# Optimization experiments

Measured on AMD Instinct MI355X. Metric: run time of the kernel, lower is better.

The kernel has to match this reference:

```python
import jax, jax.numpy as jnp
import numpy as np

N_NODES = 100000


def gcn_conv(x, edge_index, W, b):
    # PyG GCNConv: add self-loops, symmetric norm, then scatter-aggregate.
    n = x.shape[0]
    x = x @ W  # [N, out]
    src = jnp.concatenate([edge_index[0], jnp.arange(n)])  # self-loops
    dst = jnp.concatenate([edge_index[1], jnp.arange(n)])
    ones = jnp.ones(src.shape[0], dtype=x.dtype)
    deg = jax.ops.segment_sum(ones, dst, num_segments=n)  # in-degree incl. self-loops
    dis = jnp.where(deg > 0, jax.lax.rsqrt(deg), 0.0)
    norm = dis[src] * dis[dst]  # [E+N]
    msg = x[src] * norm[:, None]  # gather + scale
    out = jax.ops.segment_sum(msg, dst, num_segments=n)
    return out + b


def setup_inputs() -> dict:
    key = jax.random.key(0)
    ks = jax.random.split(key, 8)
    in_dim, h1, h2, out_dim, E = 128, 128, 64, 10, 1600000
    glorot = lambda k, fi, fo: jax.random.normal(k, (fi, fo), jnp.float32) * np.sqrt(2.0 / (fi + fo))
    return {
        "x": jax.random.normal(ks[0], (N_NODES, in_dim), jnp.float32),
        "edge_index": jax.random.randint(ks[1], (2, E), 0, N_NODES, jnp.int64),
        "W1": glorot(ks[2], in_dim, h1),
        "b1": jnp.zeros((h1,), jnp.float32),
        "W2": glorot(ks[3], h1, h2),
        "b2": jnp.zeros((h2,), jnp.float32),
        "Wf": glorot(ks[4], h2, out_dim),
        "bf": jnp.zeros((out_dim,), jnp.float32),
    }


def reference(x, edge_index, W1, b1, W2, b2, Wf, bf):
    h = jax.nn.relu(gcn_conv(x, edge_index, W1, b1))
    h = jax.nn.relu(gcn_conv(h, edge_index, W2, b2))
    logits = h @ Wf + bf
    return jax.nn.softmax(logits, axis=1)
```

## Files before the change

kernel.cpp:

```cpp
#include <hip/hip_runtime.h>
#include <math.h>

#define NN 100000
#define D_IN 128
#define D_H1 128
#define D_H2 64
#define D_O 10
#define NB 256
#define BDIV 391
#define ECH 4096
#define COLCAP 8192

static const size_t OFF_G1     = 0;
static const size_t OFF_G2     = 25600000;
static const size_t OFF_W1T    = 40000000;
static const size_t OFF_W2T    = 40100000;
static const size_t OFF_PART   = 76800000;
static const size_t OFF_COL    = 102400000;
static const size_t OFF_DIS    = 108800000;
static const size_t OFF_ROWPTR = 109300000;
static const size_t OFF_HIST   = 109800000;
static const size_t OFF_TOT    = 110700000;

typedef __attribute__((ext_vector_type(8))) short short8;
typedef __attribute__((ext_vector_type(4))) float floatx4;

__device__ inline unsigned int pack_bf2(float a, float b) {
  unsigned int ua = __float_as_uint(a);
  ua += 0x7fffu + ((ua >> 16) & 1u);
  unsigned int ub = __float_as_uint(b);
  ub += 0x7fffu + ((ub >> 16) & 1u);
  return (ua >> 16) | (ub & 0xffff0000u);
}
__device__ inline unsigned short bf16u(float a) {
  unsigned int ua = __float_as_uint(a);
  ua += 0x7fffu + ((ua >> 16) & 1u);
  return (unsigned short)(ua >> 16);
}
__device__ inline float bflo(unsigned int u) { return __uint_as_float(u << 16); }
__device__ inline float bfhi(unsigned int u) { return __uint_as_float(u & 0xffff0000u); }
__device__ inline short8 as_short8(uint4 u) {
  union { uint4 u4; short8 s8; } c; c.u4 = u; return c.s8;
}
__device__ inline void acc_u4(float* acc, uint4 u) {
  acc[0] += bflo(u.x); acc[1] += bfhi(u.x);
  acc[2] += bflo(u.y); acc[3] += bfhi(u.y);
  acc[4] += bflo(u.z); acc[5] += bfhi(u.z);
  acc[6] += bflo(u.w); acc[7] += bfhi(u.w);
}

__global__ __launch_bounds__(256) void histo_kernel(
    const int* __restrict__ dst, int* __restrict__ H, int E, int nchunk,
    const float* __restrict__ W1, const float* __restrict__ W2,
    unsigned short* __restrict__ w1t, unsigned short* __restrict__ w2t) {
  __shared__ int hist[NB];
  const int tid = threadIdx.x;
  hist[tid] = 0;
  __syncthreads();
  const int e0 = blockIdx.x * ECH;
#pragma unroll
  for (int i = 0; i < ECH / 256; ++i) {
    int e = e0 + i * 256 + tid;
    if (e < E) atomicAdd(&hist[dst[e] / BDIV], 1);
  }
  __syncthreads();
  H[tid * nchunk + blockIdx.x] = hist[tid];
  if (blockIdx.x < 64) {
    int o = blockIdx.x * 256 + tid;
    int nn = o >> 7, k = o & 127;
    w1t[o] = bf16u(W1[(size_t)k * D_H1 + nn]);
  } else if (blockIdx.x < 96) {
    int o = (blockIdx.x - 64) * 256 + tid;
    int nn = o >> 7, k = o & 127;
    w2t[o] = bf16u(W2[(size_t)k * D_H2 + nn]);
  }
}

__global__ __launch_bounds__(256) void bucket_scan_kernel(
    int* __restrict__ H, int* __restrict__ total, int nchunk) {
  __shared__ int sm[256];
  const int tid = threadIdx.x;
  int* row = H + (size_t)blockIdx.x * nchunk;
  int carry = 0;
  for (int t0 = 0; t0 < nchunk; t0 += 256) {
    int idx = t0 + tid;
    int v = (idx < nchunk) ? row[idx] : 0;
    sm[tid] = v;
    __syncthreads();
#pragma unroll
    for (int off = 1; off < 256; off <<= 1) {
      int t2 = (tid >= off) ? sm[tid - off] : 0;
      __syncthreads();
      sm[tid] += t2;
      __syncthreads();
    }
    int incl = sm[tid];
    int ttot = sm[255];
    __syncthreads();
    if (idx < nchunk) row[idx] = carry + incl - v;
    carry += ttot;
  }
  if (tid == 0) total[blockIdx.x] = carry;
}

__global__ __launch_bounds__(256) void scatter_kernel(
    const int* __restrict__ src, const int* __restrict__ dst,
    const int* __restrict__ H, const int* __restrict__ total,
    unsigned int* __restrict__ part, int E, int nchunk) {
  __shared__ int sm[NB];
  __shared__ int offs_s[NB];
  __shared__ int base_s[NB];
  __shared__ int cnt[NB];
  const int tid = threadIdx.x;
  {
    int v = total[tid];
    sm[tid] = v;
    __syncthreads();
#pragma unroll
    for (int off = 1; off < 256; off <<= 1) {
      int t2 = (tid >= off) ? sm[tid - off] : 0;
      __syncthreads();
      sm[tid] += t2;
      __syncthreads();
    }
    base_s[tid] = sm[tid] - v;
  }
  offs_s[tid] = H[tid * nchunk + blockIdx.x];
  cnt[tid] = 0;
  __syncthreads();
  const int e0 = blockIdx.x * ECH;
#pragma unroll
  for (int i = 0; i < ECH / 256; ++i) {
    int e = e0 + i * 256 + tid;
    if (e < E) {
      int d = dst[e];
      int s = src[e];
      int b = d / BDIV;
      int r = atomicAdd(&cnt[b], 1);
      unsigned int p = ((unsigned int)(d - b * BDIV) << 17) | (unsigned int)s;
      part[(size_t)base_s[b] + offs_s[b] + r] = p;
    }
  }
}

__global__ __launch_bounds__(256) void bucket_csr_kernel(
    const unsigned int* __restrict__ part, const int* __restrict__ total,
    int* __restrict__ row_ptr, float* __restrict__ dis,
    int* __restrict__ col, int n, int E) {
  __shared__ int sm[256];
  __shared__ int ldeg[BDIV + 1];
  __shared__ int lofs[BDIV + 1];
  __shared__ int col_s[COLCAP];
  __shared__ int ebase_s, ecnt_s;
  const int tid = threadIdx.x;
  const int b = blockIdx.x;
  const int lo = b * BDIV;
  const int nn = min(n - lo, BDIV);
  {
    int v = total[tid];
    sm[tid] = v;
    __syncthreads();
#pragma unroll
    for (int off = 1; off < 256; off <<= 1) {
      int t2 = (tid >= off) ? sm[tid - off] : 0;
      __syncthreads();
      sm[tid] += t2;
      __syncthreads();
    }
    if (tid == b) { ebase_s = sm[tid] - v; ecnt_s = v; }
  }
  for (int t = tid; t <= BDIV; t += 256) ldeg[t] = 0;
  __syncthreads();
  const int ebase = ebase_s;
  const int ecnt = ecnt_s;
  for (int i0 = 0; i0 < ecnt; i0 += 256) {
    int idx = i0 + tid;
    if (idx < ecnt) atomicAdd(&ldeg[part[ebase + idx] >> 17], 1);
  }
  __syncthreads();
  int carry = 0;
  for (int t0 = 0; t0 < BDIV + 1; t0 += 256) {
    int idx = t0 + tid;
    int v = (idx <= BDIV) ? ldeg[idx] : 0;
    sm[tid] = v;
    __syncthreads();
#pragma unroll
    for (int off = 1; off < 256; off <<= 1) {
      int t2 = (tid >= off) ? sm[tid - off] : 0;
      __syncthreads();
      sm[tid] += t2;
      __syncthreads();
    }
    int incl = sm[tid];
    int ttot = sm[255];
    __syncthreads();
    if (idx <= BDIV) lofs[idx] = carry + incl - v;
    carry += ttot;
  }
  __syncthreads();
  for (int t = tid; t < nn; t += 256) {
    row_ptr[lo + t] = ebase + lofs[t];
    dis[lo + t] = rsqrtf((float)ldeg[t] + 1.0f);
  }
  if (b == NB - 1 && tid == 0) row_ptr[n] = E;
  __syncthreads();
  for (int i0 = 0; i0 < ecnt; i0 += 256) {
    int idx = i0 + tid;
    if (idx < ecnt) {
      unsigned int p = part[ebase + idx];
      int r = atomicAdd(&lofs[p >> 17], 1);
      if (r < COLCAP) col_s[r] = (int)(p & 0x1FFFFu);
    }
  }
  __syncthreads();
  const int m = min(ecnt, COLCAP);
  for (int idx = tid; idx < m; idx += 256) col[ebase + idx] = col_s[idx];
}

template <int NOUT>
__global__ __launch_bounds__(256) void gemm_mfma_kernel(
    const float* __restrict__ A_, const unsigned short* __restrict__ wt,
    const float* __restrict__ dis, unsigned short* __restrict__ out, int nrows) {
  constexpr int K = 128;
  constexpr int NT = NOUT / 16;
  constexpr int LDW = K + 8;
  __shared__ unsigned short buf[4 * 16 * LDW];
  const int tid = threadIdx.x;

  const int wave = tid >> 6;
  const int lane = tid & 63;
  const int quad = lane >> 4;
  const int cg = lane & 15;
  const int row0w = blockIdx.x * 64 + wave * 16;

  short8 afr[4];
  {
    int row = row0w + cg;
    if (row > nrows - 1) row = nrows - 1;
#pragma unroll
    for (int kb = 0; kb < 4; ++kb) {
      const float* p = A_ + (size_t)row * K + kb * 32 + quad * 8;
      float4 v0 = *(const float4*)(p);
      float4 v1 = *(const float4*)(p + 4);
      uint4 u;
      u.x = pack_bf2(v0.x, v0.y); u.y = pack_bf2(v0.z, v0.w);
      u.z = pack_bf2(v1.x, v1.y); u.w = pack_bf2(v1.z, v1.w);
      afr[kb] = as_short8(u);
    }
  }

  floatx4 acc[NT];
#pragma unroll
  for (int t = 0; t < NT; ++t) acc[t] = (floatx4){0.f, 0.f, 0.f, 0.f};
#pragma unroll
  for (int t = 0; t < NT; ++t) {
    const unsigned short* wrow = wt + (size_t)(t * 16 + cg) * K;
#pragma unroll
    for (int kb = 0; kb < 4; ++kb) {
      short8 bfr = *(const short8*)(wrow + kb * 32 + quad * 8);
      acc[t] = __builtin_amdgcn_mfma_f32_16x16x32_bf16(afr[kb], bfr, acc[t], 0, 0, 0);
    }
  }

  float4 dv4 = *(const float4*)(dis + row0w + quad * 4);
  float dvs[4] = {dv4.x, dv4.y, dv4.z, dv4.w};
  unsigned short* mybuf = buf + wave * 16 * LDW;
#pragma unroll
  for (int t = 0; t < NT; ++t)
#pragma unroll
    for (int r = 0; r < 4; ++r)
      mybuf[(quad * 4 + r) * LDW + t * 16 + cg] = bf16u(acc[t][r] * dvs[r]);
  __syncthreads();

  constexpr int CHUNKS = NOUT / 8;
  constexpr int RPI = 64 / CHUNKS;
  int cid = lane % CHUNKS;
  int rs = lane / CHUNKS;
#pragma unroll
  for (int i = 0; i < 16 / RPI; ++i) {
    int r = rs + i * RPI;
    int grow = row0w + r;
    if (grow < nrows) {
      uint4 u = *(const uint4*)(mybuf + r * LDW + cid * 8);
      *(uint4*)(out + (size_t)grow * NOUT + cid * 8) = u;
    }
  }
}

__global__ __launch_bounds__(256, 8) void gather1_gemm2_kernel(
    const unsigned short* __restrict__ g, const int* __restrict__ col,
    const int* __restrict__ row_ptr, const float* __restrict__ dis,
    const float* __restrict__ b1, const unsigned short* __restrict__ w2t,
    unsigned short* __restrict__ g2, int n) {
  constexpr int K = D_H1;
  constexpr int LDW = K + 8;
  constexpr int LDO = 80;
  __shared__ unsigned short hl[16 * LDW];
  __shared__ unsigned short obuf[16 * LDO];
  const int tid = threadIdx.x;
  const int row0 = blockIdx.x * 16;

  {
    const int v = row0 + (tid >> 4);
    const int c = (tid & 15) * 8;
    const int start = row_ptr[v];
    const int end = row_ptr[v + 1];
    float acc[8];
#pragma unroll
    for (int q = 0; q < 8; ++q) acc[q] = 0.f;
    acc_u4(acc, *(const uint4*)(g + (size_t)v * K + c));
    int e = start;
    for (; e + 4 <= end; e += 4) {
      int s0 = col[e + 0], s1 = col[e + 1], s2 = col[e + 2], s3 = col[e + 3];
      uint4 u0 = *(const uint4*)(g + (size_t)s0 * K + c);
      uint4 u1 = *(const uint4*)(g + (size_t)s1 * K + c);
      uint4 u2 = *(const uint4*)(g + (size_t)s2 * K + c);
      uint4 u3 = *(const uint4*)(g + (size_t)s3 * K + c);
      acc_u4(acc, u0); acc_u4(acc, u1); acc_u4(acc, u2); acc_u4(acc, u3);
    }
    for (; e < end; ++e) {
      uint4 u = *(const uint4*)(g + (size_t)col[e] * K + c);
      acc_u4(acc, u);
    }
    float dv = dis[v];
    float4 bv0 = *(const float4*)(b1 + c);
    float4 bv1 = *(const float4*)(b1 + c + 4);
    float r0 = fmaxf(dv * acc[0] + bv0.x, 0.f);
    float r1 = fmaxf(dv * acc[1] + bv0.y, 0.f);
    float r2 = fmaxf(dv * acc[2] + bv0.z, 0.f);
    float r3 = fmaxf(dv * acc[3] + bv0.w, 0.f);
    float r4 = fmaxf(dv * acc[4] + bv1.x, 0.f);
    float r5 = fmaxf(dv * acc[5] + bv1.y, 0.f);
    float r6 = fmaxf(dv * acc[6] + bv1.z, 0.f);
    float r7 = fmaxf(dv * acc[7] + bv1.w, 0.f);
    uint4 o;
    o.x = pack_bf2(r0, r1);
    o.y = pack_bf2(r2, r3);
    o.z = pack_bf2(r4, r5);
    o.w = pack_bf2(r6, r7);
    *(uint4*)(hl + (tid >> 4) * LDW + c) = o;
  }
  __syncthreads();

  {
    const int wave = tid >> 6;
    const int lane = tid & 63;
    const int quad = lane >> 4;
    const int cg = lane & 15;
    floatx4 acc = (floatx4){0.f, 0.f, 0.f, 0.f};
    const unsigned short* wrow = w2t + (size_t)(wave * 16 + cg) * K;
    const unsigned short* arow = hl + cg * LDW;
#pragma unroll
    for (int kb = 0; kb < 4; ++kb) {
      short8 afr = *(const short8*)(arow + kb * 32 + quad * 8);
      short8 bfr = *(const short8*)(wrow + kb * 32 + quad * 8);
      acc = __builtin_amdgcn_mfma_f32_16x16x32_bf16(afr, bfr, acc, 0, 0, 0);
    }
    float4 dv4 = *(const float4*)(dis + row0 + quad * 4);
    float dvs[4] = {dv4.x, dv4.y, dv4.z, dv4.w};
#pragma unroll
    for (int r = 0; r < 4; ++r)
      obuf[(quad * 4 + r) * LDO + wave * 16 + cg] = bf16u(acc[r] * dvs[r]);
  }
  __syncthreads();

  if (tid < 128) {
    int r = tid >> 3;
    int cid = tid & 7;
    uint4 u = *(const uint4*)(obuf + r * LDO + cid * 8);
    *(uint4*)(g2 + (size_t)(row0 + r) * D_H2 + cid * 8) = u;
  }
}

__global__ __launch_bounds__(256) void gather2_final_kernel(
    const unsigned short* __restrict__ g, const int* __restrict__ col,
    const int* __restrict__ row_ptr, const float* __restrict__ dis,
    const float* __restrict__ b2, const float* __restrict__ Wf,
    const float* __restrict__ bf, float* __restrict__ out, int n) {
  constexpr int LDH = 72;
  __shared__ unsigned short ha[32 * LDH];
  __shared__ unsigned short wtf[16 * LDH];
  __shared__ float bfs[D_O];
  __shared__ float ls[32][12];
  const int tid = threadIdx.x;
  if (tid < 128) {
    int nn = tid >> 3;
    int k = (tid & 7) * 8;
    uint4 u;
    if (nn < D_O) {
      u.x = pack_bf2(Wf[(size_t)(k + 0) * D_O + nn], Wf[(size_t)(k + 1) * D_O + nn]);
      u.y = pack_bf2(Wf[(size_t)(k + 2) * D_O + nn], Wf[(size_t)(k + 3) * D_O + nn]);
      u.z = pack_bf2(Wf[(size_t)(k + 4) * D_O + nn], Wf[(size_t)(k + 5) * D_O + nn]);
      u.w = pack_bf2(Wf[(size_t)(k + 6) * D_O + nn], Wf[(size_t)(k + 7) * D_O + nn]);
    } else {
      u = make_uint4(0u, 0u, 0u, 0u);
    }
    *(uint4*)(wtf + nn * LDH + k) = u;
  }
  if (tid < D_O) bfs[tid] = bf[tid];

  const int gid = blockIdx.x * 256 + tid;
  const int v = gid >> 3;
  const int nl = tid >> 3;
  const int c = (tid & 7) * 8;
  if (v < n) {
    int start = row_ptr[v];
    int end = row_ptr[v + 1];
    float acc[8];
#pragma unroll
    for (int q = 0; q < 8; ++q) acc[q] = 0.f;
    acc_u4(acc, *(const uint4*)(g + (size_t)v * D_H2 + c));
    int e = start;
    for (; e + 4 <= end; e += 4) {
      int s0 = col[e + 0], s1 = col[e + 1], s2 = col[e + 2], s3 = col[e + 3];
      uint4 u0 = *(const uint4*)(g + (size_t)s0 * D_H2 + c);
      uint4 u1 = *(const uint4*)(g + (size_t)s1 * D_H2 + c);
      uint4 u2 = *(const uint4*)(g + (size_t)s2 * D_H2 + c);
      uint4 u3 = *(const uint4*)(g + (size_t)s3 * D_H2 + c);
      acc_u4(acc, u0); acc_u4(acc, u1); acc_u4(acc, u2); acc_u4(acc, u3);
    }
    for (; e < end; ++e) {
      uint4 u = *(const uint4*)(g + (size_t)col[e] * D_H2 + c);
      acc_u4(acc, u);
    }
    float dv = dis[v];
    float4 bv0 = *(const float4*)(b2 + c);
    float4 bv1 = *(const float4*)(b2 + c + 4);
    float r0 = fmaxf(dv * acc[0] + bv0.x, 0.f);
    float r1 = fmaxf(dv * acc[1] + bv0.y, 0.f);
    float r2 = fmaxf(dv * acc[2] + bv0.z, 0.f);
    float r3 = fmaxf(dv * acc[3] + bv0.w, 0.f);
    float r4 = fmaxf(dv * acc[4] + bv1.x, 0.f);
    float r5 = fmaxf(dv * acc[5] + bv1.y, 0.f);
    float r6 = fmaxf(dv * acc[6] + bv1.z, 0.f);
    float r7 = fmaxf(dv * acc[7] + bv1.w, 0.f);
    uint4 o;
    o.x = pack_bf2(r0, r1);
    o.y = pack_bf2(r2, r3);
    o.z = pack_bf2(r4, r5);
    o.w = pack_bf2(r6, r7);
    *(uint4*)(ha + nl * LDH + c) = o;
  }
  __syncthreads();
  {
    const int wave = tid >> 6;
    if (wave < 2) {
      const int lane = tid & 63;
      const int quad = lane >> 4;
      const int cg = lane & 15;
      floatx4 acc = (floatx4){0.f, 0.f, 0.f, 0.f};
      const unsigned short* arow = ha + (wave * 16 + cg) * LDH;
      const unsigned short* wrow = wtf + cg * LDH;
#pragma unroll
      for (int kb = 0; kb < 2; ++kb) {
        short8 afr = *(const short8*)(arow + kb * 32 + quad * 8);
        short8 bfr = *(const short8*)(wrow + kb * 32 + quad * 8);
        acc = __builtin_amdgcn_mfma_f32_16x16x32_bf16(afr, bfr, acc, 0, 0, 0);
      }
      if (cg < D_O) {
        float bb = bfs[cg];
#pragma unroll
        for (int r = 0; r < 4; ++r)
          ls[wave * 16 + quad * 4 + r][cg] = acc[r] + bb;
      }
    }
  }
  __syncthreads();
  if (tid < 32) {
    int v2 = blockIdx.x * 32 + tid;
    if (v2 < n) {
      float m = ls[tid][0];
#pragma unroll
      for (int j = 1; j < D_O; ++j) m = fmaxf(m, ls[tid][j]);
      float s = 0.f;
      float ex[D_O];
#pragma unroll
      for (int j = 0; j < D_O; ++j) { ex[j] = expf(ls[tid][j] - m); s += ex[j]; }
      float inv = 1.0f / s;
#pragma unroll
      for (int j = 0; j < D_O; ++j) ls[tid][j] = ex[j] * inv;
    }
  }
  __syncthreads();
  for (int idx = tid; idx < 32 * D_O; idx += 256) {
    int gidx = blockIdx.x * 32 * D_O + idx;
    if (gidx < n * D_O) out[gidx] = ls[idx / D_O][idx % D_O];
  }
}

extern "C" void kernel_launch(void* const* d_in, const int* in_sizes, int n_in,
                              void* d_out, int out_size, void* d_ws, size_t ws_size,
                              hipStream_t stream) {
  const float* x  = (const float*)d_in[0];
  const int*   ei = (const int*)d_in[1];
  const float* W1 = (const float*)d_in[2];
  const float* b1 = (const float*)d_in[3];
  const float* W2 = (const float*)d_in[4];
  const float* b2 = (const float*)d_in[5];
  const float* Wf = (const float*)d_in[6];
  const float* bf = (const float*)d_in[7];
  float* out = (float*)d_out;

  const int E = in_sizes[1] / 2;
  const int* src = ei;
  const int* dst = ei + E;

  char* ws = (char*)d_ws;
  unsigned short* g1 = (unsigned short*)(ws + OFF_G1);
  unsigned short* g2 = (unsigned short*)(ws + OFF_G2);
  unsigned short* w1t = (unsigned short*)(ws + OFF_W1T);
  unsigned short* w2t = (unsigned short*)(ws + OFF_W2T);
  unsigned int* part = (unsigned int*)(ws + OFF_PART);
  int*   col     = (int*)(ws + OFF_COL);
  float* dis     = (float*)(ws + OFF_DIS);
  int*   row_ptr = (int*)(ws + OFF_ROWPTR);
  int*   H       = (int*)(ws + OFF_HIST);
  int*   total   = (int*)(ws + OFF_TOT);

  const int nchunk = (E + ECH - 1) / ECH;

  histo_kernel<<<nchunk, 256, 0, stream>>>(dst, H, E, nchunk, W1, W2, w1t, w2t);
  bucket_scan_kernel<<<NB, 256, 0, stream>>>(H, total, nchunk);
  scatter_kernel<<<nchunk, 256, 0, stream>>>(src, dst, H, total, part, E, nchunk);
  bucket_csr_kernel<<<NB, 256, 0, stream>>>(part, total, row_ptr, dis, col, NN, E);

  gemm_mfma_kernel<D_H1>
      <<<(NN + 63) / 64, 256, 0, stream>>>(x, w1t, dis, g1, NN);

  gather1_gemm2_kernel<<<NN / 16, 256, 0, stream>>>(
      g1, col, row_ptr, dis, b1, w2t, g2, NN);

  gather2_final_kernel<<<(NN + 31) / 32, 256, 0, stream>>>(
      g2, col, row_ptr, dis, b2, Wf, bf, out, NN);
}
```

Baseline: 264.3 us.

## Sort CSR columns by source segment and stage weights in LDS for GEMMs

```diff
diff --git a/kernel.cpp b/kernel.cpp
--- a/kernel.cpp
+++ b/kernel.cpp
@@ -10,6 +10,8 @@
 #define BDIV 391
 #define ECH 4096
 #define COLCAP 8192
+#define S_SEG 16
+#define SEGW 6250
 
 static const size_t OFF_G1     = 0;
 static const size_t OFF_G2     = 25600000;
@@ -147,10 +149,11 @@
     const unsigned int* __restrict__ part, const int* __restrict__ total,
     int* __restrict__ row_ptr, float* __restrict__ dis,
     int* __restrict__ col, int n, int E) {
+  constexpr int TOT = BDIV * S_SEG;
   __shared__ int sm[256];
-  __shared__ int ldeg[BDIV + 1];
-  __shared__ int lofs[BDIV + 1];
+  __shared__ int cnt2[TOT + 1];
   __shared__ int col_s[COLCAP];
+  __shared__ int wsum[4];
   __shared__ int ebase_s, ecnt_s;
   const int tid = threadIdx.x;
   const int b = blockIdx.x;
@@ -169,38 +172,59 @@
     }
     if (tid == b) { ebase_s = sm[tid] - v; ecnt_s = v; }
   }
-  for (int t = tid; t <= BDIV; t += 256) ldeg[t] = 0;
+  for (int t = tid; t <= TOT; t += 256) cnt2[t] = 0;
   __syncthreads();
   const int ebase = ebase_s;
   const int ecnt = ecnt_s;
   for (int i0 = 0; i0 < ecnt; i0 += 256) {
     int idx = i0 + tid;
-    if (idx < ecnt) atomicAdd(&ldeg[part[ebase + idx] >> 17], 1);
-  }
-  __syncthreads();
-  int carry = 0;
-  for (int t0 = 0; t0 < BDIV + 1; t0 += 256) {
-    int idx = t0 + tid;
-    int v = (idx <= BDIV) ? ldeg[idx] : 0;
-    sm[tid] = v;
-    __syncthreads();
-#pragma unroll
-    for (int off = 1; off < 256; off <<= 1) {
-      int t2 = (tid >= off) ? sm[tid - off] : 0;
-      __syncthreads();
-      sm[tid] += t2;
-      __syncthreads();
-    }
-    int incl = sm[tid];
-    int ttot = sm[255];
-    __syncthreads();
-    if (idx <= BDIV) lofs[idx] = carry + incl - v;
-    carry += ttot;
+    if (idx < ecnt) {
+      unsigned int p = part[ebase + idx];
+      int s = (int)(p & 0x1FFFFu);
+      atomicAdd(&cnt2[(int)(p >> 17) * S_SEG + s / SEGW], 1);
+    }
+  }
+  __syncthreads();
+  {
+    const int lane = tid & 63;
+    const int wv = tid >> 6;
+    int carry = 0;
+    for (int t0 = 0; t0 < TOT; t0 += 1024) {
+      int i0 = t0 + tid * 4;
+      int v0 = (i0 + 0 < TOT) ? cnt2[i0 + 0] : 0;
+      int v1 = (i0 + 1 < TOT) ? cnt2[i0 + 1] : 0;
+      int v2 = (i0 + 2 < TOT) ? cnt2[i0 + 2] : 0;
+      int v3 = (i0 + 3 < TOT) ? cnt2[i0 + 3] : 0;
+      int ts = v0 + v1 + v2 + v3;
+      int incl = ts;
+#pragma unroll
+      for (int off = 1; off < 64; off <<= 1) {
+        int o = __shfl_up(incl, off);
+        if (lane >= off) incl += o;
+      }
+      if (lane == 63) wsum[wv] = incl;
+      __syncthreads();
+      int wpre = 0;
+#pragma unroll
+      for (int w = 0; w < 4; ++w)
+        if (w < wv) wpre += wsum[w];
+      int btot = wsum[0] + wsum[1] + wsum[2] + wsum[3];
+      int e = carry + wpre + (incl - ts);
+      __syncthreads();
+      if (i0 + 0 < TOT) cnt2[i0 + 0] = e;
+      if (i0 + 1 < TOT) cnt2[i0 + 1] = e + v0;
+      if (i0 + 2 < TOT) cnt2[i0 + 2] = e + v0 + v1;
+      if (i0 + 3 < TOT) cnt2[i0 + 3] = e + v0 + v1 + v2;
+      carry += btot;
+    }
+    if (tid == 0) cnt2[TOT] = carry;
   }
   __syncthreads();
   for (int t = tid; t < nn; t += 256) {
-    row_ptr[lo + t] = ebase + lofs[t];
-    dis[lo + t] = rsqrtf((float)ldeg[t] + 1.0f);
+    int b0 = cnt2[t * S_SEG];
+    int b1 = cnt2[(t + 1) * S_SEG];
+    row_ptr[lo + t] = ebase + b0;
+    dis[lo + t] = rsqrtf((float)(b1 - b0) + 1.0f);
   }
   if (b == NB - 1 && tid == 0) row_ptr[n] = E;
   __syncthreads();
@@ -208,8 +232,9 @@
     int idx = i0 + tid;
     if (idx < ecnt) {
       unsigned int p = part[ebase + idx];
-      int r = atomicAdd(&lofs[p >> 17], 1);
-      if (r < COLCAP) col_s[r] = (int)(p & 0x1FFFFu);
+      int s = (int)(p & 0x1FFFFu);
+      int r = atomicAdd(&cnt2[(int)(p >> 17) * S_SEG + s / SEGW], 1);
+      if (r < COLCAP) col_s[r] = s;
     }
   }
   __syncthreads();
@@ -219,13 +244,25 @@
 
 template <int NOUT>
 __global__ __launch_bounds__(256) void gemm_mfma_kernel(
-    const float* __restrict__ A_, const unsigned short* __restrict__ wt,
+    const float* __restrict__ A_, const unsigned short* __restrict__ w1t,
     const float* __restrict__ dis, unsigned short* __restrict__ out, int nrows) {
   constexpr int K = 128;
   constexpr int NT = NOUT / 16;
   constexpr int LDW = K + 8;
-  __shared__ unsigned short buf[4 * 16 * LDW];
-  const int tid = threadIdx.x;
+  __shared__ unsigned short wt[NOUT * LDW];
+  unsigned short* buf = wt;
+  const int tid = threadIdx.x;
+
+  {
+    const uint4* wsrc = (const uint4*)w1t;
+#pragma unroll
+    for (int j = 0; j < NOUT * K / (8 * 256); ++j) {
+      int o = tid + j * 256;
+      int row = o >> 4;
+      int k8 = (o & 15) * 8;
+      *(uint4*)(wt + row * LDW + k8) = wsrc[o];
+    }
+  }
 
   const int wave = tid >> 6;
   const int lane = tid & 63;
@@ -248,19 +285,21 @@
       afr[kb] = as_short8(u);
     }
   }
+  __syncthreads();
 
   floatx4 acc[NT];
 #pragma unroll
   for (int t = 0; t < NT; ++t) acc[t] = (floatx4){0.f, 0.f, 0.f, 0.f};
 #pragma unroll
   for (int t = 0; t < NT; ++t) {
-    const unsigned short* wrow = wt + (size_t)(t * 16 + cg) * K;
+    const unsigned short* wrow = wt + (t * 16 + cg) * LDW;
 #pragma unroll
     for (int kb = 0; kb < 4; ++kb) {
       short8 bfr = *(const short8*)(wrow + kb * 32 + quad * 8);
       acc[t] = __builtin_amdgcn_mfma_f32_16x16x32_bf16(afr[kb], bfr, acc[t], 0, 0, 0);
     }
   }
+  __syncthreads();
 
   float4 dv4 = *(const float4*)(dis + row0w + quad * 4);
   float dvs[4] = {dv4.x, dv4.y, dv4.z, dv4.w};
@@ -287,7 +326,7 @@
   }
 }
 
-__global__ __launch_bounds__(256, 8) void gather1_gemm2_kernel(
+__global__ __launch_bounds__(256) void gather1_gemm2_kernel(
     const unsigned short* __restrict__ g, const int* __restrict__ col,
     const int* __restrict__ row_ptr, const float* __restrict__ dis,
     const float* __restrict__ b1, const unsigned short* __restrict__ w2t,
@@ -295,10 +334,22 @@
   constexpr int K = D_H1;
   constexpr int LDW = K + 8;
   constexpr int LDO = 80;
+  __shared__ unsigned short wt[D_H2 * LDW];
   __shared__ unsigned short hl[16 * LDW];
   __shared__ unsigned short obuf[16 * LDO];
   const int tid = threadIdx.x;
   const int row0 = blockIdx.x * 16;
+
+  {
+    const uint4* wsrc = (const uint4*)w2t;
+#pragma unroll
+    for (int j = 0; j < 4; ++j) {
+      int o = tid + j * 256;
+      int row = o >> 4;
+      int k8 = (o & 15) * 8;
+      *(uint4*)(wt + row * LDW + k8) = wsrc[o];
+    }
+  }
 
   {
     const int v = row0 + (tid >> 4);
@@ -348,7 +399,7 @@
     const int quad = lane >> 4;
     const int cg = lane & 15;
     floatx4 acc = (floatx4){0.f, 0.f, 0.f, 0.f};
-    const unsigned short* wrow = w2t + (size_t)(wave * 16 + cg) * K;
+    const unsigned short* wrow = wt + (wave * 16 + cg) * LDW;
     const unsigned short* arow = hl + cg * LDW;
 #pragma unroll
     for (int kb = 0; kb < 4; ++kb) {
```

Result: faster. 243.9 us (-7.7%).
